# Kernel tuning notes

Measured on AMD Instinct MI355X. Metric: run time of the kernel, lower is better.

The kernel has to match this reference:

```python
import jax, jax.numpy as jnp
import numpy as np

FUZZYNUM = 4
EPS = 1e-5  # torch BatchNorm2d default


def conv2d(x, w, b):
    y = jax.lax.conv_general_dilated(x, w, (1, 1), 'SAME',
                                     dimension_numbers=('NCHW', 'OIHW', 'NCHW'))
    return y + b[None, :, None, None]


def batchnorm(x, gamma, beta):
    # training-mode BN: batch statistics over (N,H,W), biased variance
    m = jnp.mean(x, axis=(0, 2, 3), keepdims=True)
    v = jnp.mean((x - m) ** 2, axis=(0, 2, 3), keepdims=True)
    xn = (x - m) * jax.lax.rsqrt(v + EPS)
    return xn * gamma[None, :, None, None] + beta[None, :, None, None]


def fuzzify(x, lb_all, ub_all):
    # x: (N,1,H,W) -- conv1 output has 1 channel, so only bounds[0, f] are used.
    # Per-f sequential semantics of the original loop (x is mutated across f):
    #  in-range (ld>0 & ud>0): add exp(-0.5 ld^2)+exp(-0.5 ud^2)
    #  out-of-range (ld<0 or ud<0): reflect x -> 2*lb - x, then add
    #      exp(-0.5 ld^2) + exp(-0.5 (ub - x_new)^2)
    #  (the other sub-branches in the source are mathematically unreachable)
    fuzz = jnp.zeros_like(x)
    for f in range(FUZZYNUM):
        lb = lb_all[0, f]
        ub = ub_all[0, f]
        ld = x - lb
        ud = ub - x
        in_range = (ld > 0) & (ud > 0)
        out_range = (ld < 0) | (ud < 0)
        x_ref = 2.0 * lb - x
        c_in = jnp.exp(-0.5 * ld ** 2) + jnp.exp(-0.5 * ud ** 2)
        c_out = jnp.exp(-0.5 * ld ** 2) + jnp.exp(-0.5 * (ub - x_ref) ** 2)
        fuzz = fuzz + jnp.where(in_range, c_in, jnp.where(out_range, c_out, 0.0))
        x = jnp.where(out_range, x_ref, x)
    return fuzz


def setup_inputs() -> dict:
    key = jax.random.key(0)
    k0, k1, k2 = jax.random.split(key, 3)
    N, C, H, W = 16, 64, 256, 256
    sigma, init_mean = 2.0, 0.2
    x = jax.random.normal(k0, (N, C, H, W), dtype=jnp.float32)
    bnd1 = 1.0 / np.sqrt(C * 9)
    bnd2 = 1.0 / np.sqrt(1 * 9)
    conv1_w = jax.random.uniform(k1, (1, C, 3, 3), jnp.float32, -bnd1, bnd1)
    conv2_w = jax.random.uniform(k2, (C, 1, 3, 3), jnp.float32, -bnd2, bnd2)
    center = jnp.full((C, FUZZYNUM), init_mean, jnp.float32)
    return {
        'x': x,
        'conv1_w': conv1_w,
        'conv1_b': jnp.zeros((1,), jnp.float32),
        'conv2_w': conv2_w,
        'conv2_b': jnp.zeros((C,), jnp.float32),
        'bn1_g': jnp.ones((1,), jnp.float32),
        'bn1_b': jnp.zeros((1,), jnp.float32),
        'bn2_g': jnp.ones((C,), jnp.float32),
        'bn2_b': jnp.zeros((C,), jnp.float32),
        'lower_bound': center - sigma,
        'upper_bound': center + sigma,
    }


def reference(x, conv1_w, conv1_b, conv2_w, conv2_b, bn1_g, bn1_b, bn2_g, bn2_b,
              lower_bound, upper_bound):
    h = batchnorm(conv2d(x, conv1_w, conv1_b), bn1_g, bn1_b)  # (N,1,H,W)
    fz = fuzzify(h, lower_bound, upper_bound)                  # (N,1,H,W)
    return batchnorm(conv2d(fz, conv2_w, conv2_b), bn2_g, bn2_b)  # (N,C,H,W)
```

## Files before the change

### kernel.cpp

```cpp
#include <hip/hip_runtime.h>
#include <cstdint>

#define EPS 1e-5f
#define INV_NTOT (1.0f / 1048576.0f)

#define FZ_OFF  1048576
#define ST_OFF  2097152

__device__ __forceinline__ void dev_atomic_add(float* p, float v) {
    __hip_atomic_fetch_add(p, v, __ATOMIC_RELAXED, __HIP_MEMORY_SCOPE_AGENT);
}

__global__ __launch_bounds__(512) void k1_conv1(
    const float* __restrict__ x, const float* __restrict__ w1,
    float* __restrict__ h0, float* __restrict__ stats)
{
    __shared__ float tile[10][264];
    __shared__ float red_s[8], red_q[8];

    const int tid   = threadIdx.x;
    const int bid   = blockIdx.x;
    const int n     = bid >> 5;
    const int ht    = bid & 31;
    const int h0b   = ht << 3;

    const int t     = tid & 255;
    const int ohb   = (tid >> 8) << 2;
    const int rs    = tid >> 6;
    const int col4  = (tid & 63) << 2;

    float acc0 = 0.f, acc1 = 0.f, acc2 = 0.f, acc3 = 0.f;

    if (tid < 10) { tile[tid][3] = 0.f; tile[tid][260] = 0.f; }

    const float* xn = x + ((size_t)n << 22);

    for (int c = 0; c < 64; ++c) {
        __syncthreads();
        {
            int g = h0b - 1 + rs;
            float4 v = make_float4(0.f, 0.f, 0.f, 0.f);
            if ((unsigned)g < 256u)
                v = *(const float4*)(xn + ((size_t)c << 16) + (g << 8) + col4);
            *(float4*)&tile[rs][4 + col4] = v;
            if (rs < 2) {
                int g2 = h0b + 7 + rs;
                float4 v2 = make_float4(0.f, 0.f, 0.f, 0.f);
                if ((unsigned)g2 < 256u)
                    v2 = *(const float4*)(xn + ((size_t)c << 16) + (g2 << 8) + col4);
                *(float4*)&tile[8 + rs][4 + col4] = v2;
            }
        }
        __syncthreads();

        float wc[9];
        #pragma unroll
        for (int k = 0; k < 9; ++k) wc[k] = w1[c * 9 + k];

        #pragma unroll
        for (int rr = 0; rr < 6; ++rr) {
            const int sr = ohb + rr;
            float vm = tile[sr][3 + t];
            float v0 = tile[sr][4 + t];
            float vp = tile[sr][5 + t];
            #pragma unroll
            for (int di = 0; di < 3; ++di) {
                const int l = rr - di;
                if (l >= 0 && l < 4) {
                    float contrib = wc[di * 3 + 0] * vm + wc[di * 3 + 1] * v0
                                  + wc[di * 3 + 2] * vp;
                    if      (l == 0) acc0 += contrib;
                    else if (l == 1) acc1 += contrib;
                    else if (l == 2) acc2 += contrib;
                    else             acc3 += contrib;
                }
            }
        }
    }

    size_t ob = ((size_t)n << 16) + (size_t)((h0b + ohb) << 8) + t;
    h0[ob]       = acc0;
    h0[ob + 256] = acc1;
    h0[ob + 512] = acc2;
    h0[ob + 768] = acc3;

    float s  = acc0 + acc1 + acc2 + acc3;
    float sq = acc0 * acc0 + acc1 * acc1 + acc2 * acc2 + acc3 * acc3;
    #pragma unroll
    for (int o = 32; o > 0; o >>= 1) {
        s  += __shfl_down(s,  o, 64);
        sq += __shfl_down(sq, o, 64);
    }
    const int wave = tid >> 6, lane = tid & 63;
    if (lane == 0) { red_s[wave] = s; red_q[wave] = sq; }
    __syncthreads();
    if (tid == 0) {
        float S = 0.f, Q = 0.f;
        #pragma unroll
        for (int i = 0; i < 8; ++i) { S += red_s[i]; Q += red_q[i]; }
        dev_atomic_add(&stats[0], S);
        dev_atomic_add(&stats[1], Q);
    }
}

__global__ __launch_bounds__(256) void k3_fuzzify(
    const float* __restrict__ h0, const float* __restrict__ stats,
    const float* __restrict__ bn1_g, const float* __restrict__ bn1_b,
    const float* __restrict__ lb, const float* __restrict__ ub,
    float* __restrict__ fz)
{
    const int i = blockIdx.x * 256 + threadIdx.x;

    const float mean = stats[0] * INV_NTOT;
    const float var  = stats[1] * INV_NTOT - mean * mean;
    const float rstd = rsqrtf(var + EPS);
    const float A    = bn1_g[0] * rstd;
    const float B    = bn1_b[0] - mean * A;

    float lbv[4], ubv[4];
    #pragma unroll
    for (int f = 0; f < 4; ++f) { lbv[f] = lb[f]; ubv[f] = ub[f]; }

    float4 hv = *(const float4*)(h0 + (size_t)i * 4);
    float in[4] = { hv.x, hv.y, hv.z, hv.w };
    float res[4];
    #pragma unroll
    for (int k = 0; k < 4; ++k) {
        float xv = A * in[k] + B;
        float fuzz = 0.f;
        #pragma unroll
        for (int f = 0; f < 4; ++f) {
            float ld = xv - lbv[f];
            float ud = ubv[f] - xv;
            bool inr  = (ld > 0.f) && (ud > 0.f);
            bool outr = (ld < 0.f) || (ud < 0.f);
            float xr  = 2.f * lbv[f] - xv;
            float u2  = ubv[f] - xr;
            float e1  = __expf(-0.5f * ld * ld);
            float cin  = e1 + __expf(-0.5f * ud * ud);
            float cout = e1 + __expf(-0.5f * u2 * u2);
            fuzz += inr ? cin : (outr ? cout : 0.f);
            xv = outr ? xr : xv;
        }
        res[k] = fuzz;
    }
    *(float4*)(fz + (size_t)i * 4) = make_float4(res[0], res[1], res[2], res[3]);
}

__global__ __launch_bounds__(256) void k4_stats(
    const float* __restrict__ fz, float* __restrict__ stats)
{
    float s9[9], q45[45];
    #pragma unroll
    for (int i = 0; i < 9; ++i)  s9[i]  = 0.f;
    #pragma unroll
    for (int i = 0; i < 45; ++i) q45[i] = 0.f;

    const int base = blockIdx.x * 256 + threadIdx.x;
    for (int k = 0; k < 16; ++k) {
        int p = base + k * 65536;
        int w = p & 255, h = (p >> 8) & 255, n = p >> 16;
        const float* f = fz + ((size_t)n << 16);
        float v[9];
        #pragma unroll
        for (int di = 0; di < 3; ++di)
            #pragma unroll
            for (int dj = 0; dj < 3; ++dj) {
                int hh = h + di - 1, ww = w + dj - 1;
                v[di * 3 + dj] = ((unsigned)hh < 256u && (unsigned)ww < 256u)
                               ? f[(hh << 8) + ww] : 0.f;
            }
        int idx = 0;
        #pragma unroll
        for (int a = 0; a < 9; ++a) {
            s9[a] += v[a];
            #pragma unroll
            for (int b = a; b < 9; ++b) q45[idx++] += v[a] * v[b];
        }
    }

    __shared__ float red[4][54];
    const int wave = threadIdx.x >> 6, lane = threadIdx.x & 63;
    float vals[54];
    #pragma unroll
    for (int i = 0; i < 9; ++i)  vals[i]     = s9[i];
    #pragma unroll
    for (int i = 0; i < 45; ++i) vals[9 + i] = q45[i];
    #pragma unroll
    for (int i = 0; i < 54; ++i) {
        float vv = vals[i];
        #pragma unroll
        for (int o = 32; o > 0; o >>= 1) vv += __shfl_down(vv, o, 64);
        if (lane == 0) red[wave][i] = vv;
    }
    __syncthreads();
    if (threadIdx.x < 54) {
        float tot = red[0][threadIdx.x] + red[1][threadIdx.x]
                  + red[2][threadIdx.x] + red[3][threadIdx.x];
        dev_atomic_add(&stats[2 + threadIdx.x], tot);
    }
}

__global__ void k5_finalize(
    const float* __restrict__ w2, const float* __restrict__ bn2_g,
    const float* __restrict__ bn2_b, float* __restrict__ stats)
{
    const int c = threadIdx.x;
    if (c >= 64) return;
    float w[9];
    #pragma unroll
    for (int k = 0; k < 9; ++k) w[k] = w2[c * 9 + k];
    float P = 0.f;
    #pragma unroll
    for (int k = 0; k < 9; ++k) P += w[k] * stats[2 + k];
    P *= INV_NTOT;
    float QF = 0.f;
    int idx = 0;
    #pragma unroll
    for (int a = 0; a < 9; ++a)
        #pragma unroll
        for (int b = a; b < 9; ++b) {
            float qv = stats[11 + idx]; idx++;
            QF += w[a] * w[b] * qv * ((a == b) ? 1.f : 2.f);
        }
    QF *= INV_NTOT;
    float var   = QF - P * P;
    float scale = bn2_g[c] * rsqrtf(var + EPS);
    float bias  = bn2_b[c] - P * scale;
    stats[56 + c]  = scale;
    stats[120 + c] = bias;
}

__global__ __launch_bounds__(256) void k6_conv2(
    const float* __restrict__ fz, const float* __restrict__ w2,
    const float* __restrict__ stats, float* __restrict__ out)
{
    __shared__ float tile[34][36];
    const int bid = blockIdx.x;
    const int n   = bid >> 6;
    const int th  = (bid >> 3) & 7;
    const int tw  = bid & 7;
    const int h0b = th << 5, w0b = tw << 5;
    const int tid = threadIdx.x;

    const float* f = fz + ((size_t)n << 16);
    for (int i = tid; i < 34 * 34; i += 256) {
        int rr = i / 34, cc = i - rr * 34;
        int gh = h0b + rr - 1, gw = w0b + cc - 1;
        tile[rr][cc] = ((unsigned)gh < 256u && (unsigned)gw < 256u)
                     ? f[(gh << 8) + gw] : 0.f;
    }
    __syncthreads();

    const int r = tid >> 3, q = tid & 7;
    float v[3][6];
    #pragma unroll
    for (int di = 0; di < 3; ++di)
        #pragma unroll
        for (int j = 0; j < 6; ++j)
            v[di][j] = tile[r + di][(q << 2) + j];

    const size_t ob = ((size_t)n << 22) + (size_t)((h0b + r) << 8) + w0b + (q << 2);
    for (int c = 0; c < 64; ++c) {
        float wk[9];
        #pragma unroll
        for (int k = 0; k < 9; ++k) wk[k] = w2[c * 9 + k];
        const float sc = stats[56 + c], bi = stats[120 + c];
        float4 o;
        float* op = &o.x;
        #pragma unroll
        for (int k = 0; k < 4; ++k) {
            float y = 0.f;
            #pragma unroll
            for (int di = 0; di < 3; ++di)
                y += wk[di * 3 + 0] * v[di][k]
                   + wk[di * 3 + 1] * v[di][k + 1]
                   + wk[di * 3 + 2] * v[di][k + 2];
            op[k] = y * sc + bi;
        }
        *(float4*)(out + ob + ((size_t)c << 16)) = o;
    }
}

extern "C" void kernel_launch(void* const* d_in, const int* in_sizes, int n_in,
                              void* d_out, int out_size, void* d_ws, size_t ws_size,
                              hipStream_t stream)
{
    const float* x  = (const float*)d_in[0];
    const float* w1 = (const float*)d_in[1];
    const float* w2 = (const float*)d_in[3];
    const float* g1 = (const float*)d_in[5];
    const float* b1 = (const float*)d_in[6];
    const float* g2 = (const float*)d_in[7];
    const float* b2 = (const float*)d_in[8];
    const float* lb = (const float*)d_in[9];
    const float* ub = (const float*)d_in[10];

    float* ws  = (float*)d_ws;
    float* h0  = ws;
    float* fz  = ws + FZ_OFF;
    float* st  = ws + ST_OFF;
    float* out = (float*)d_out;

    hipMemsetAsync(st, 0, 56 * sizeof(float), stream);
    k1_conv1  <<<dim3(512),  dim3(512), 0, stream>>>(x, w1, h0, st);
    k3_fuzzify<<<dim3(1024), dim3(256), 0, stream>>>(h0, st, g1, b1, lb, ub, fz);
    k4_stats  <<<dim3(256),  dim3(256), 0, stream>>>(fz, st);
    k5_finalize<<<dim3(1),   dim3(64),  0, stream>>>(w2, g2, b2, st);
    k6_conv2  <<<dim3(1024), dim3(256), 0, stream>>>(fz, w2, st, out);
}
```

Measured before the change: 566.9 us.

## Restructure conv1 per-wave channel split, fuse BN2 finalize into conv2, nontemporal stores

conv1 no longer stages each input channel through shared memory with two barriers per channel. Each wave now owns 8 channels, reads its rows directly from global memory, gets the horizontal neighbours by cross-lane shuffles, and accumulates 8 output rows. A shared-memory reduction across waves then produces the output rows. The separate one-block BN2 finalize kernel is removed, and every conv2 block recomputes the 64 scale and bias values into shared memory, trading one launch for redundant per-block work. conv2 output stores become nontemporal, and the conv2 tile is padded to reduce bank conflicts.

```diff
diff --git a/kernel.cpp b/kernel.cpp
--- a/kernel.cpp
+++ b/kernel.cpp
@@ -4,6 +4,8 @@
 #define EPS 1e-5f
 #define INV_NTOT (1.0f / 1048576.0f)
 
+typedef float f4_vec __attribute__((ext_vector_type(4)));
+
 #define FZ_OFF  1048576
 #define ST_OFF  2097152
 
@@ -11,88 +13,91 @@
     __hip_atomic_fetch_add(p, v, __ATOMIC_RELAXED, __HIP_MEMORY_SCOPE_AGENT);
 }
 
-__global__ __launch_bounds__(512) void k1_conv1(
+__global__ __launch_bounds__(512, 4) void k1_conv1(
     const float* __restrict__ x, const float* __restrict__ w1,
     float* __restrict__ h0, float* __restrict__ stats)
 {
-    __shared__ float tile[10][264];
+    __shared__ float part[8][4][256];
     __shared__ float red_s[8], red_q[8];
 
-    const int tid   = threadIdx.x;
-    const int bid   = blockIdx.x;
-    const int n     = bid >> 5;
-    const int ht    = bid & 31;
-    const int h0b   = ht << 3;
-
-    const int t     = tid & 255;
-    const int ohb   = (tid >> 8) << 2;
-    const int rs    = tid >> 6;
-    const int col4  = (tid & 63) << 2;
-
-    float acc0 = 0.f, acc1 = 0.f, acc2 = 0.f, acc3 = 0.f;
-
-    if (tid < 10) { tile[tid][3] = 0.f; tile[tid][260] = 0.f; }
-
-    const float* xn = x + ((size_t)n << 22);
-
-    for (int c = 0; c < 64; ++c) {
-        __syncthreads();
-        {
-            int g = h0b - 1 + rs;
+    const int tid  = threadIdx.x;
+    const int wv   = tid >> 6;
+    const int lane = tid & 63;
+
+    const int b   = blockIdx.x;
+    const int lin = ((b & 7) << 6) + (b >> 3);
+    const int n   = lin >> 5;
+    const int h0b = (lin & 31) << 3;
+
+    float acc[8][4];
+    #pragma unroll
+    for (int o = 0; o < 8; ++o)
+        #pragma unroll
+        for (int k = 0; k < 4; ++k) acc[o][k] = 0.f;
+
+    const float* xn = x + ((size_t)n << 22) + ((size_t)(wv << 3) << 16)
+                    + (lane << 2);
+
+    for (int cc = 0; cc < 8; ++cc) {
+        const float* wcp = w1 + ((wv << 3) + cc) * 9;
+        float wc[9];
+        #pragma unroll
+        for (int k = 0; k < 9; ++k) wc[k] = wcp[k];
+        const float* xc = xn + ((size_t)cc << 16);
+
+        #pragma unroll
+        for (int r = -1; r <= 8; ++r) {
+            const int g = h0b + r;
             float4 v = make_float4(0.f, 0.f, 0.f, 0.f);
-            if ((unsigned)g < 256u)
-                v = *(const float4*)(xn + ((size_t)c << 16) + (g << 8) + col4);
-            *(float4*)&tile[rs][4 + col4] = v;
-            if (rs < 2) {
-                int g2 = h0b + 7 + rs;
-                float4 v2 = make_float4(0.f, 0.f, 0.f, 0.f);
-                if ((unsigned)g2 < 256u)
-                    v2 = *(const float4*)(xn + ((size_t)c << 16) + (g2 << 8) + col4);
-                *(float4*)&tile[8 + rs][4 + col4] = v2;
-            }
-        }
-        __syncthreads();
-
-        float wc[9];
-        #pragma unroll
-        for (int k = 0; k < 9; ++k) wc[k] = w1[c * 9 + k];
-
-        #pragma unroll
-        for (int rr = 0; rr < 6; ++rr) {
-            const int sr = ohb + rr;
-            float vm = tile[sr][3 + t];
-            float v0 = tile[sr][4 + t];
-            float vp = tile[sr][5 + t];
+            if ((unsigned)g < 256u) v = *(const float4*)(xc + (g << 8));
+            float lf = __shfl_up(v.w, 1, 64);
+            float rt = __shfl_down(v.x, 1, 64);
+            if (lane == 0)  lf = 0.f;
+            if (lane == 63) rt = 0.f;
             #pragma unroll
             for (int di = 0; di < 3; ++di) {
-                const int l = rr - di;
-                if (l >= 0 && l < 4) {
-                    float contrib = wc[di * 3 + 0] * vm + wc[di * 3 + 1] * v0
-                                  + wc[di * 3 + 2] * vp;
-                    if      (l == 0) acc0 += contrib;
-                    else if (l == 1) acc1 += contrib;
-                    else if (l == 2) acc2 += contrib;
-                    else             acc3 += contrib;
+                const int o = r + 1 - di;
+                if (o >= 0 && o < 8) {
+                    const float w0 = wc[di * 3 + 0];
+                    const float w1v = wc[di * 3 + 1];
+                    const float w2v = wc[di * 3 + 2];
+                    acc[o][0] += w0 * lf  + w1v * v.x + w2v * v.y;
+                    acc[o][1] += w0 * v.x + w1v * v.y + w2v * v.z;
+                    acc[o][2] += w0 * v.y + w1v * v.z + w2v * v.w;
+                    acc[o][3] += w0 * v.z + w1v * v.w + w2v * rt;
                 }
             }
         }
     }
 
-    size_t ob = ((size_t)n << 16) + (size_t)((h0b + ohb) << 8) + t;
-    h0[ob]       = acc0;
-    h0[ob + 256] = acc1;
-    h0[ob + 512] = acc2;
-    h0[ob + 768] = acc3;
-
-    float s  = acc0 + acc1 + acc2 + acc3;
-    float sq = acc0 * acc0 + acc1 * acc1 + acc2 * acc2 + acc3 * acc3;
+    float s = 0.f, sq = 0.f;
+    #pragma unroll
+    for (int half = 0; half < 2; ++half) {
+        __syncthreads();
+        #pragma unroll
+        for (int o = 0; o < 4; ++o)
+            *(float4*)&part[wv][o][lane << 2] = *(float4*)acc[(half << 2) + o];
+        __syncthreads();
+        #pragma unroll
+        for (int k = 0; k < 2; ++k) {
+            const int idx = tid + (k << 9);
+            const int ro  = idx >> 8;
+            const int co  = idx & 255;
+            float v = 0.f;
+            #pragma unroll
+            for (int w = 0; w < 8; ++w) v += part[w][ro][co];
+            h0[((size_t)n << 16) + ((size_t)(h0b + (half << 2) + ro) << 8) + co] = v;
+            s  += v;
+            sq += v * v;
+        }
+    }
+
     #pragma unroll
     for (int o = 32; o > 0; o >>= 1) {
         s  += __shfl_down(s,  o, 64);
         sq += __shfl_down(sq, o, 64);
     }
-    const int wave = tid >> 6, lane = tid & 63;
-    if (lane == 0) { red_s[wave] = s; red_q[wave] = sq; }
+    if (lane == 0) { red_s[wv] = s; red_q[wv] = sq; }
     __syncthreads();
     if (tid == 0) {
         float S = 0.f, Q = 0.f;
@@ -201,41 +206,13 @@
     }
 }
 
-__global__ void k5_finalize(
-    const float* __restrict__ w2, const float* __restrict__ bn2_g,
-    const float* __restrict__ bn2_b, float* __restrict__ stats)
-{
-    const int c = threadIdx.x;
-    if (c >= 64) return;
-    float w[9];
-    #pragma unroll
-    for (int k = 0; k < 9; ++k) w[k] = w2[c * 9 + k];
-    float P = 0.f;
-    #pragma unroll
-    for (int k = 0; k < 9; ++k) P += w[k] * stats[2 + k];
-    P *= INV_NTOT;
-    float QF = 0.f;
-    int idx = 0;
-    #pragma unroll
-    for (int a = 0; a < 9; ++a)
-        #pragma unroll
-        for (int b = a; b < 9; ++b) {
-            float qv = stats[11 + idx]; idx++;
-            QF += w[a] * w[b] * qv * ((a == b) ? 1.f : 2.f);
-        }
-    QF *= INV_NTOT;
-    float var   = QF - P * P;
-    float scale = bn2_g[c] * rsqrtf(var + EPS);
-    float bias  = bn2_b[c] - P * scale;
-    stats[56 + c]  = scale;
-    stats[120 + c] = bias;
-}
-
 __global__ __launch_bounds__(256) void k6_conv2(
     const float* __restrict__ fz, const float* __restrict__ w2,
+    const float* __restrict__ bn2_g, const float* __restrict__ bn2_b,
     const float* __restrict__ stats, float* __restrict__ out)
 {
-    __shared__ float tile[34][36];
+    __shared__ float tile[34][37];
+    __shared__ float sc_s[64], bi_s[64];
     const int bid = blockIdx.x;
     const int n   = bid >> 6;
     const int th  = (bid >> 3) & 7;
@@ -250,6 +227,31 @@
         tile[rr][cc] = ((unsigned)gh < 256u && (unsigned)gw < 256u)
                      ? f[(gh << 8) + gw] : 0.f;
     }
+
+    if (tid < 64) {
+        const int c = tid;
+        float w[9];
+        #pragma unroll
+        for (int k = 0; k < 9; ++k) w[k] = w2[c * 9 + k];
+        float P = 0.f;
+        #pragma unroll
+        for (int k = 0; k < 9; ++k) P += w[k] * stats[2 + k];
+        P *= INV_NTOT;
+        float QF = 0.f;
+        int idx = 0;
+        #pragma unroll
+        for (int a = 0; a < 9; ++a)
+            #pragma unroll
+            for (int bb = a; bb < 9; ++bb) {
+                float qv = stats[11 + idx]; idx++;
+                QF += w[a] * w[bb] * qv * ((a == bb) ? 1.f : 2.f);
+            }
+        QF *= INV_NTOT;
+        float varc  = QF - P * P;
+        float scale = bn2_g[c] * rsqrtf(varc + EPS);
+        sc_s[c] = scale;
+        bi_s[c] = bn2_b[c] - P * scale;
+    }
     __syncthreads();
 
     const int r = tid >> 3, q = tid & 7;
@@ -265,9 +267,8 @@
         float wk[9];
         #pragma unroll
         for (int k = 0; k < 9; ++k) wk[k] = w2[c * 9 + k];
-        const float sc = stats[56 + c], bi = stats[120 + c];
-        float4 o;
-        float* op = &o.x;
+        const float sc = sc_s[c], bi = bi_s[c];
+        f4_vec o;
         #pragma unroll
         for (int k = 0; k < 4; ++k) {
             float y = 0.f;
@@ -276,9 +277,9 @@
                 y += wk[di * 3 + 0] * v[di][k]
                    + wk[di * 3 + 1] * v[di][k + 1]
                    + wk[di * 3 + 2] * v[di][k + 2];
-            op[k] = y * sc + bi;
-        }
-        *(float4*)(out + ob + ((size_t)c << 16)) = o;
+            o[k] = y * sc + bi;
+        }
+        __builtin_nontemporal_store(o, (f4_vec*)(out + ob + ((size_t)c << 16)));
     }
 }
 
@@ -306,6 +307,5 @@
     k1_conv1  <<<dim3(512),  dim3(512), 0, stream>>>(x, w1, h0, st);
     k3_fuzzify<<<dim3(1024), dim3(256), 0, stream>>>(h0, st, g1, b1, lb, ub, fz);
     k4_stats  <<<dim3(256),  dim3(256), 0, stream>>>(fz, st);
-    k5_finalize<<<dim3(1),   dim3(64),  0, stream>>>(w2, g2, b2, st);
-    k6_conv2  <<<dim3(1024), dim3(256), 0, stream>>>(fz, w2, st, out);
-}
+    k6_conv2  <<<dim3(1024), dim3(256), 0, stream>>>(fz, w2, g2, b2, st, out);
+}
```

New measurement: 502.0 us. 11.4% less time.
